# Optimization experiments

Hardware: AMD Instinct MI355X
Metric: run time of the kernel (lower is better)

The kernel has to match this reference:

```python
import jax, jax.numpy as jnp
import numpy as np

B, K = 4, 128
V_IN, V_OUT = 256, 256
E_IN, E_OUT = 512, 512
P_PE, T_PE = 200, 100
HEADS = 16  # c_atten_head


def _lin(key, din, dout):
    kw, kb = jax.random.split(key)
    W = jax.random.normal(kw, (din, dout), jnp.float32) / np.sqrt(din).astype(np.float32)
    b = jax.random.normal(kb, (dout,), jnp.float32) * 0.01
    return W, b


def setup_inputs() -> dict:
    key = jax.random.key(0)
    ks = jax.random.split(key, 14)
    v_f = jax.random.normal(ks[0], (B, K, V_IN), jnp.float32)
    e_f = jax.random.normal(ks[1], (B, K * K, E_IN), jnp.float32)
    p_pe = jax.random.normal(ks[2], (B, K, P_PE), jnp.float32)
    t_pe = jax.random.normal(ks[3], (B, T_PE), jnp.float32)
    e_agg_mask = (jax.random.uniform(ks[4], (B, K, K)) > 0.1).astype(jnp.float32)
    v_agg_mask = (jax.random.uniform(ks[5], (B, K)) > 0.1).astype(jnp.float32)
    W_vpe, b_vpe = _lin(ks[6], V_IN + P_PE + T_PE, V_IN)
    W_epe, b_epe = _lin(ks[7], E_IN + T_PE, E_IN)
    W_ev1, b_ev1 = _lin(ks[8], E_IN + 2 * V_IN, E_OUT)
    W_ev2, b_ev2 = _lin(ks[9], E_OUT, E_OUT)
    W_q, b_q = _lin(ks[10], V_IN, E_OUT)
    W_k, b_k = _lin(ks[11], V_IN, E_OUT)
    W_self, b_self = _lin(ks[12], V_IN, E_OUT)
    W_out, b_out = _lin(ks[13], 2 * E_OUT, V_OUT)
    return dict(v_f=v_f, e_f=e_f, p_pe=p_pe, t_pe=t_pe,
                e_agg_mask=e_agg_mask, v_agg_mask=v_agg_mask,
                W_vpe=W_vpe, b_vpe=b_vpe, W_epe=W_epe, b_epe=b_epe,
                W_ev1=W_ev1, b_ev1=b_ev1, W_ev2=W_ev2, b_ev2=b_ev2,
                W_q=W_q, b_q=b_q, W_k=W_k, b_k=b_k,
                W_self=W_self, b_self=b_self, W_out=W_out, b_out=b_out)


def reference(v_f, e_f, p_pe, t_pe, e_agg_mask, v_agg_mask,
              W_vpe, b_vpe, W_epe, b_epe, W_ev1, b_ev1, W_ev2, b_ev2,
              W_q, b_q, W_k, b_k, W_self, b_self, W_out, b_out):
    silu = jax.nn.silu
    # PE binding
    t_v = jnp.broadcast_to(t_pe[:, None, :], (B, K, T_PE))
    v = silu(jnp.concatenate([v_f, p_pe, t_v], -1) @ W_vpe + b_vpe)          # (B,K,V_IN)
    t_e = jnp.broadcast_to(t_pe[:, None, :], (B, K * K, T_PE))
    e = silu(jnp.concatenate([e_f, t_e], -1) @ W_epe + b_epe)                # (B,K*K,E_IN)
    # dense all-pairs node features -> edge values
    pair = jnp.concatenate([jnp.broadcast_to(v[:, :, None, :], (B, K, K, V_IN)),
                            jnp.broadcast_to(v[:, None, :, :], (B, K, K, V_IN))], -1)
    ev_in = jnp.concatenate([pair.reshape(B, K * K, 2 * V_IN), e], -1)
    e_value = silu(ev_in @ W_ev1 + b_ev1) @ W_ev2 + b_ev2                     # (B,K*K,E_OUT)
    agg_e = e_value.reshape(B, K, K, E_OUT)
    # elementwise-multiply / head-sum attention
    q = v @ W_q + b_q                                                         # (B,K,E_OUT)
    k = v @ W_k + b_k
    att = (q[:, :, None, :] * k[:, None, :, :]).reshape(B, K, K, E_OUT // HEADS, HEADS)
    att = att.sum(-1, keepdims=True) / np.float32(np.sqrt(HEADS * 3.0))       # (B,K,K,G,1)
    a = jax.nn.sigmoid(att) * e_agg_mask[..., None, None]
    a = a / (a.sum(2, keepdims=True) + 1e-6)
    a = jnp.broadcast_to(a, (B, K, K, E_OUT // HEADS, HEADS)).reshape(B, K, K, E_OUT)
    agg_v = (a * agg_e).sum(2)                                                # (B,K,E_OUT)
    v2 = agg_v + silu(v @ W_self + b_self)
    # masked max-pool over nodes
    pooled = (v2 - 1e9 * (1.0 - v_agg_mask)[..., None]).max(1, keepdims=True)
    pooled = jnp.broadcast_to(pooled, (B, K, E_OUT))
    v_out = silu(jnp.concatenate([v2, pooled], -1) @ W_out + b_out)           # (B,K,V_OUT)
    return v_out, e_value
```

## Files before the change

kernel.cpp:

```cpp
#include <hip/hip_runtime.h>

typedef unsigned short ushort_t;
typedef __attribute__((ext_vector_type(8))) short bf16x8;
typedef __attribute__((ext_vector_type(4))) float f32x4;

__device__ __forceinline__ ushort_t f2bf(float f) {
    union { float f; unsigned u; } v; v.f = f;
    unsigned r = v.u + 0x7FFFu + ((v.u >> 16) & 1u);
    return (ushort_t)(r >> 16);
}
__device__ __forceinline__ float siluf(float x) { return x / (1.f + __expf(-x)); }
__device__ __forceinline__ float sigm(float x)  { return 1.f / (1.f + __expf(-x)); }

__device__ __forceinline__ void gl2lds16(const void* g, void* l) {
    __builtin_amdgcn_global_load_lds(
        (__attribute__((address_space(1))) void*)(const_cast<void*>(g)),
        (__attribute__((address_space(3))) void*)(l), 16, 0, 0);
}

__device__ __forceinline__ size_t wts_off(int n, int k) {
    return (size_t)((k >> 5) * 16384) + n * 32
         + ((((k >> 3) & 3) ^ (n & 3)) * 8) + (k & 7);
}

__global__ void k_pt(const float* W_epe, const float* W_ev1, const float* W_ev2,
                     const float* t_pe, const float* W_vpe, const float* b_vpe,
                     const float* b_epe,
                     ushort_t* WT_epe, ushort_t* WT_c, ushort_t* WT_ev2,
                     float* c_v, float* c_e) {
    int n = blockIdx.x, mat = blockIdx.y, t = threadIdx.x;
    if (mat == 3) {
        if (n < 4) {
            int b = n;
            for (int col = t; col < 512; col += 256) {
                float acc = b_epe[col];
                for (int u = 0; u < 100; ++u) acc += t_pe[b*100+u] * W_epe[(512+u)*512 + col];
                c_e[b*512 + col] = acc;
            }
            {
                float acc = b_vpe[t];
                for (int u = 0; u < 100; ++u) acc += t_pe[b*100+u] * W_vpe[(456+u)*256 + t];
                c_v[b*256 + t] = acc;
            }
        }
        return;
    }
    const float* src; ushort_t* dst;
    if (mat == 0)      { src = W_epe;            dst = WT_epe; }
    else if (mat == 1) { src = W_ev1 + 512*512;  dst = WT_c;   }
    else               { src = W_ev2;            dst = WT_ev2; }
    for (int k = t; k < 512; k += 256)
        dst[wts_off(n, k)] = f2bf(src[k*512 + n]);
}

__global__ void k_node_v(const float* v_f, const float* p_pe, const float* W_vpe,
                         const float* c_v, float* v) {
    __shared__ float rv[4][256];
    __shared__ float rp[4][200];
    int r0 = blockIdx.x * 4, t = threadIdx.x;
    for (int rr = 0; rr < 4; ++rr) {
        rv[rr][t] = v_f[(r0+rr)*256 + t];
        if (t < 200) rp[rr][t] = p_pe[(r0+rr)*200 + t];
    }
    __syncthreads();
    int b = r0 >> 7;
    float acc[4];
    float cv = c_v[b*256 + t];
    for (int rr = 0; rr < 4; ++rr) acc[rr] = cv;
    for (int k = 0; k < 256; ++k) {
        float w = W_vpe[k*256 + t];
        #pragma unroll
        for (int rr = 0; rr < 4; ++rr) acc[rr] += rv[rr][k] * w;
    }
    for (int k = 0; k < 200; ++k) {
        float w = W_vpe[(256+k)*256 + t];
        #pragma unroll
        for (int rr = 0; rr < 4; ++rr) acc[rr] += rp[rr][k] * w;
    }
    for (int rr = 0; rr < 4; ++rr) v[(r0+rr)*256 + t] = siluf(acc[rr]);
}

__global__ void k_node_proj(const float* v,
                            const float* W_q, const float* b_q,
                            const float* W_k, const float* b_k,
                            const float* W_self, const float* b_self,
                            const float* W_ev1, const float* b_ev1,
                            float* q, float* kk, float* vs, float* P, float* Q) {
    __shared__ float rv[4][256];
    int r0 = blockIdx.x * 4, which = blockIdx.y, t = threadIdx.x;
    for (int rr = 0; rr < 4; ++rr) rv[rr][t] = v[(r0+rr)*256 + t];
    __syncthreads();
    const float* W; const float* bias = nullptr; float* out; bool do_silu = false;
    if (which == 0)      { W = W_q;    bias = b_q;    out = q;  }
    else if (which == 1) { W = W_k;    bias = b_k;    out = kk; }
    else if (which == 2) { W = W_self; bias = b_self; out = vs; do_silu = true; }
    else if (which == 3) { W = W_ev1;  bias = b_ev1;  out = P;  }
    else                 { W = W_ev1 + 256*512;       out = Q;  }
    float acc[4][2] = {};
    for (int k = 0; k < 256; ++k) {
        float w0 = W[k*512 + t];
        float w1 = W[k*512 + t + 256];
        #pragma unroll
        for (int rr = 0; rr < 4; ++rr) {
            acc[rr][0] += rv[rr][k] * w0;
            acc[rr][1] += rv[rr][k] * w1;
        }
    }
    float bb0 = bias ? bias[t] : 0.f;
    float bb1 = bias ? bias[t + 256] : 0.f;
    for (int rr = 0; rr < 4; ++rr) {
        float x0 = acc[rr][0] + bb0;
        float x1 = acc[rr][1] + bb1;
        if (do_silu) { x0 = siluf(x0); x1 = siluf(x1); }
        out[(r0+rr)*512 + t]       = x0;
        out[(r0+rr)*512 + t + 256] = x1;
    }
}

__global__ __launch_bounds__(256) void k_attw(const float* q, const float* kmat,
                                              const float* emask, float* anorm) {
    int bi = blockIdx.x; int b = bi >> 7, i = bi & 127;
    int t = threadIdx.x;
    __shared__ __align__(16) float qrow[512];
    __shared__ float s[128][33];
    __shared__ float invd[32];
    qrow[t]       = q[(size_t)bi*512 + t];
    qrow[t + 256] = q[(size_t)bi*512 + t + 256];
    __syncthreads();
    {
        int j = t >> 1, g0 = (t & 1) * 16;
        const float* kr = kmat + ((size_t)b*128 + j) * 512;
        float msk = emask[(size_t)b*16384 + i*128 + j];
        for (int gg = 0; gg < 16; ++gg) {
            int g = g0 + gg;
            const float4* k4 = (const float4*)(kr + g*16);
            const float4* q4 = (const float4*)(qrow + g*16);
            float acc = 0.f;
            #pragma unroll
            for (int c = 0; c < 4; ++c) {
                float4 kv = k4[c], qv = q4[c];
                acc += kv.x*qv.x + kv.y*qv.y + kv.z*qv.z + kv.w*qv.w;
            }
            s[j][g] = sigm(acc * 0.14433756729740645f) * msk;
        }
    }
    __syncthreads();
    if (t < 32) {
        float d = 1e-6f;
        for (int j = 0; j < 128; ++j) d += s[j][t];
        invd[t] = 1.f / d;
    }
    __syncthreads();
    float* dst = anorm + (size_t)bi * 4096;
    for (int idx = t; idx < 4096; idx += 256) {
        int j = idx >> 5, g = idx & 31;
        dst[idx] = s[j][g] * invd[g];
    }
}


#define MFMA(A, B, C) __builtin_amdgcn_mfma_f32_16x16x32_bf16((A), (B), (C), 0, 0, 0)

#define ISSUE(W, SL) do {                                                     \
    const ushort_t* wsrc = (W) + (size_t)(SL) * 16384 + wv * 512 + lane * 8;  \
    ushort_t* wdst = bL + ((SL) & 1) * 16384 + wv * 512;                      \
    gl2lds16(wsrc,         wdst);                                             \
    gl2lds16(wsrc + 4096,  wdst + 4096);                                      \
    gl2lds16(wsrc + 8192,  wdst + 8192);                                      \
    gl2lds16(wsrc + 12288, wdst + 12288);                                     \
} while (0)

#define COMPUTE(SL) do {                                                      \
    const ushort_t* sA = aL + (SL) * 2048;                                    \
    const ushort_t* sB = bL + ((SL) & 1) * 16384;                             \
    bf16x8 a0 = *(const bf16x8*)(sA + (ml) * 32 + qs);                        \
    bf16x8 a1 = *(const bf16x8*)(sA + (16 + ml) * 32 + qs);                   \
    bf16x8 a2 = *(const bf16x8*)(sA + (32 + ml) * 32 + qs);                   \
    bf16x8 a3 = *(const bf16x8*)(sA + (48 + ml) * 32 + qs);                   \
    bf16x8 b0 = *(const bf16x8*)(sB + (wn + ml) * 32 + qs);                   \
    bf16x8 b1 = *(const bf16x8*)(sB + (wn + 16 + ml) * 32 + qs);              \
    bf16x8 b2 = *(const bf16x8*)(sB + (wn + 32 + ml) * 32 + qs);              \
    bf16x8 b3 = *(const bf16x8*)(sB + (wn + 48 + ml) * 32 + qs);              \
    acc00 = MFMA(a0, b0, acc00); acc01 = MFMA(a0, b1, acc01);                 \
    acc02 = MFMA(a0, b2, acc02); acc03 = MFMA(a0, b3, acc03);                 \
    acc10 = MFMA(a1, b0, acc10); acc11 = MFMA(a1, b1, acc11);                 \
    acc12 = MFMA(a1, b2, acc12); acc13 = MFMA(a1, b3, acc13);                 \
    acc20 = MFMA(a2, b0, acc20); acc21 = MFMA(a2, b1, acc21);                 \
    acc22 = MFMA(a2, b2, acc22); acc23 = MFMA(a2, b3, acc23);                 \
    acc30 = MFMA(a3, b0, acc30); acc31 = MFMA(a3, b1, acc31);                 \
    acc32 = MFMA(a3, b2, acc32); acc33 = MFMA(a3, b3, acc33);                 \
} while (0)

#define RING(W) do {                                                          \
    for (int sl = 0; sl < 16; ++sl) {                                         \
        if (sl < 15) ISSUE((W), sl + 1);                                      \
        COMPUTE(sl);                                                          \
        __syncthreads();                                                      \
    }                                                                         \
} while (0)

#define EPI0(TM, TN, ACC, CV) {                                               \
    int c  = wn + (TN) * 16 + ml;                                             \
    int cb = (c >> 5) * 2048 + (c & 7);                                       \
    int cx = (c >> 3) & 3;                                                    \
    int j0 = (TM) * 16 + quad * 4;                                            \
    aL[cb + (j0+0)*32 + ((cx ^ 0) * 8)] = f2bf(siluf(ACC[0] + (CV)));         \
    aL[cb + (j0+1)*32 + ((cx ^ 1) * 8)] = f2bf(siluf(ACC[1] + (CV)));         \
    aL[cb + (j0+2)*32 + ((cx ^ 2) * 8)] = f2bf(siluf(ACC[2] + (CV)));         \
    aL[cb + (j0+3)*32 + ((cx ^ 3) * 8)] = f2bf(siluf(ACC[3] + (CV)));         \
    ACC = zero4; }

#define EPI1(TM, TN, ACC, PV) {                                               \
    int c  = wn + (TN) * 16 + ml;                                             \
    int cb = (c >> 5) * 2048 + (c & 7);                                       \
    int cx = (c >> 3) & 3;                                                    \
    int j0 = (TM) * 16 + quad * 4;                                            \
    const float* qp = Qbuf + (size_t)(b_ * 128 + half * 64 + j0) * 512 + c;   \
    aL[cb + (j0+0)*32 + ((cx ^ 0) * 8)] = f2bf(siluf(ACC[0] + (PV) + qp[0]));    \
    aL[cb + (j0+1)*32 + ((cx ^ 1) * 8)] = f2bf(siluf(ACC[1] + (PV) + qp[512]));  \
    aL[cb + (j0+2)*32 + ((cx ^ 2) * 8)] = f2bf(siluf(ACC[2] + (PV) + qp[1024])); \
    aL[cb + (j0+3)*32 + ((cx ^ 3) * 8)] = f2bf(siluf(ACC[3] + (PV) + qp[1536])); \
    ACC = zero4; }

#define EPI2(TM, TN, ACC, BV, PART) {                                         \
    int c  = wn + (TN) * 16 + ml;                                             \
    int g  = c >> 4;                                                          \
    int j0 = (TM) * 16 + quad * 4;                                            \
    float* op = out_e + (size_t)(r0 + j0) * 512 + c;                          \
    float x0 = ACC[0] + (BV); op[0]    = x0; PART += awl[(j0+0)*32 + g] * x0; \
    float x1 = ACC[1] + (BV); op[512]  = x1; PART += awl[(j0+1)*32 + g] * x1; \
    float x2 = ACC[2] + (BV); op[1024] = x2; PART += awl[(j0+2)*32 + g] * x2; \
    float x3 = ACC[3] + (BV); op[1536] = x3; PART += awl[(j0+3)*32 + g] * x3; }

__global__ __launch_bounds__(512) void k_chain(const float* ef,
                                               const ushort_t* W0, const ushort_t* W1,
                                               const ushort_t* W2,
                                               const float* c_e, const float* Pbuf,
                                               const float* Qbuf, const float* b_ev2,
                                               const float* anorm,
                                               float* out_e, float* v2buf) {
    __shared__ __align__(16) ushort_t smem[65536];
    int lin = blockIdx.x;
    int mt = (lin & 7) * 128 + (lin >> 3);
    int r0 = mt * 64;
    int bi = mt >> 1;
    int b_ = mt >> 8;
    int half = mt & 1;
    int t = threadIdx.x;
    int wv = t >> 6, lane = t & 63;
    int wn = wv * 64;
    int ml = lane & 15, quad = lane >> 4;
    int qs = (quad ^ (ml & 3)) * 8;

    const f32x4 zero4 = {0.f, 0.f, 0.f, 0.f};
    f32x4 acc00 = zero4, acc01 = zero4, acc02 = zero4, acc03 = zero4;
    f32x4 acc10 = zero4, acc11 = zero4, acc12 = zero4, acc13 = zero4;
    f32x4 acc20 = zero4, acc21 = zero4, acc22 = zero4, acc23 = zero4;
    f32x4 acc30 = zero4, acc31 = zero4, acc32 = zero4, acc33 = zero4;

    ushort_t* aL = smem;
    ushort_t* bL = smem + 32768;

    ISSUE(W0, 0);
    for (int i = 0; i < 16; ++i) {
        int qd  = i * 512 + t;
        int row = qd >> 7, k4 = (qd & 127) * 4;
        float4 f4 = *(const float4*)(ef + (size_t)(r0 + row) * 512 + k4);
        ushort_t* d = aL + (k4 >> 5) * 2048 + row * 32
                    + ((((k4 >> 3) & 3) ^ (row & 3)) * 8) + (k4 & 7);
        *(ushort4*)d = make_ushort4(f2bf(f4.x), f2bf(f4.y), f2bf(f4.z), f2bf(f4.w));
    }
    __syncthreads();
    RING(W0);
    {
        float cv0 = c_e[b_ * 512 + wn +  0 + ml];
        float cv1 = c_e[b_ * 512 + wn + 16 + ml];
        float cv2 = c_e[b_ * 512 + wn + 32 + ml];
        float cv3 = c_e[b_ * 512 + wn + 48 + ml];
        EPI0(0,0,acc00,cv0) EPI0(0,1,acc01,cv1) EPI0(0,2,acc02,cv2) EPI0(0,3,acc03,cv3)
        EPI0(1,0,acc10,cv0) EPI0(1,1,acc11,cv1) EPI0(1,2,acc12,cv2) EPI0(1,3,acc13,cv3)
        EPI0(2,0,acc20,cv0) EPI0(2,1,acc21,cv1) EPI0(2,2,acc22,cv2) EPI0(2,3,acc23,cv3)
        EPI0(3,0,acc30,cv0) EPI0(3,1,acc31,cv1) EPI0(3,2,acc32,cv2) EPI0(3,3,acc33,cv3)
    }
    ISSUE(W1, 0);
    __syncthreads();
    RING(W1);
    {
        float Pv0 = Pbuf[(size_t)bi * 512 + wn +  0 + ml];
        float Pv1 = Pbuf[(size_t)bi * 512 + wn + 16 + ml];
        float Pv2 = Pbuf[(size_t)bi * 512 + wn + 32 + ml];
        float Pv3 = Pbuf[(size_t)bi * 512 + wn + 48 + ml];
        EPI1(0,0,acc00,Pv0) EPI1(0,1,acc01,Pv1) EPI1(0,2,acc02,Pv2) EPI1(0,3,acc03,Pv3)
        EPI1(1,0,acc10,Pv0) EPI1(1,1,acc11,Pv1) EPI1(1,2,acc12,Pv2) EPI1(1,3,acc13,Pv3)
        EPI1(2,0,acc20,Pv0) EPI1(2,1,acc21,Pv1) EPI1(2,2,acc22,Pv2) EPI1(2,3,acc23,Pv3)
        EPI1(3,0,acc30,Pv0) EPI1(3,1,acc31,Pv1) EPI1(3,2,acc32,Pv2) EPI1(3,3,acc33,Pv3)
    }
    ISSUE(W2, 0);
    __syncthreads();
    RING(W2);
    {
        float* awl = (float*)bL;
        ((float4*)awl)[t] = ((const float4*)(anorm + (size_t)bi * 4096 + half * 2048))[t];
        __syncthreads();
        float bv0 = b_ev2[wn +  0 + ml];
        float bv1 = b_ev2[wn + 16 + ml];
        float bv2 = b_ev2[wn + 32 + ml];
        float bv3 = b_ev2[wn + 48 + ml];
        float p0 = 0.f, p1 = 0.f, p2 = 0.f, p3 = 0.f;
        EPI2(0,0,acc00,bv0,p0) EPI2(0,1,acc01,bv1,p1) EPI2(0,2,acc02,bv2,p2) EPI2(0,3,acc03,bv3,p3)
        EPI2(1,0,acc10,bv0,p0) EPI2(1,1,acc11,bv1,p1) EPI2(1,2,acc12,bv2,p2) EPI2(1,3,acc13,bv3,p3)
        EPI2(2,0,acc20,bv0,p0) EPI2(2,1,acc21,bv1,p1) EPI2(2,2,acc22,bv2,p2) EPI2(2,3,acc23,bv3,p3)
        EPI2(3,0,acc30,bv0,p0) EPI2(3,1,acc31,bv1,p1) EPI2(3,2,acc32,bv2,p2) EPI2(3,3,acc33,bv3,p3)
        { float p = p0; p += __shfl_down(p, 32); p += __shfl_down(p, 16);
          if (lane < 16) atomicAdd(v2buf + (size_t)bi * 512 + wn +  0 + ml, p); }
        { float p = p1; p += __shfl_down(p, 32); p += __shfl_down(p, 16);
          if (lane < 16) atomicAdd(v2buf + (size_t)bi * 512 + wn + 16 + ml, p); }
        { float p = p2; p += __shfl_down(p, 32); p += __shfl_down(p, 16);
          if (lane < 16) atomicAdd(v2buf + (size_t)bi * 512 + wn + 32 + ml, p); }
        { float p = p3; p += __shfl_down(p, 32); p += __shfl_down(p, 16);
          if (lane < 16) atomicAdd(v2buf + (size_t)bi * 512 + wn + 48 + ml, p); }
    }
}

__global__ __launch_bounds__(1024) void k_out(const float* v2, const float* vmask,
                                              const float* W_out, const float* b_out,
                                              float* out) {
    __shared__ float rv[2][512];
    __shared__ float vm[128];
    __shared__ float pm[2][512];
    __shared__ float pooled[512];
    __shared__ float red[2][2][256];
    __shared__ float cpred[2][256];
    int t = threadIdx.x;
    int r0 = blockIdx.x * 2, b = r0 >> 7;
    if (t < 128) vm[t] = -1e9f * (1.f - vmask[b*128 + t]);
    rv[t >> 9][t & 511] = v2[(size_t)(r0 + (t >> 9)) * 512 + (t & 511)];
    __syncthreads();
    {
        int col = t & 511, rc = t >> 9;
        int i0 = rc * 64;
        const float* src = v2 + ((size_t)(b*128 + i0)) * 512 + col;
        float m = -1e30f;
        #pragma unroll 8
        for (int i = 0; i < 64; ++i)
            m = fmaxf(m, src[(size_t)i * 512] + vm[i0 + i]);
        pm[rc][col] = m;
    }
    __syncthreads();
    if (t < 512) pooled[t] = fmaxf(pm[0][t], pm[1][t]);
    __syncthreads();
    {
        int col = t & 255, kc = t >> 8;
        if (kc < 2) {
            int k0 = kc * 256;
            float a0 = 0.f, a1 = 0.f;
            #pragma unroll 8
            for (int k = 0; k < 256; ++k) {
                float w = W_out[(size_t)(k0 + k) * 256 + col];
                a0 += rv[0][k0 + k] * w;
                a1 += rv[1][k0 + k] * w;
            }
            red[kc][0][col] = a0;
            red[kc][1][col] = a1;
        } else {
            int d0 = (kc - 2) * 256;
            float cp = 0.f;
            #pragma unroll 8
            for (int d = 0; d < 256; ++d)
                cp += pooled[d0 + d] * W_out[(size_t)(512 + d0 + d) * 256 + col];
            cpred[kc - 2][col] = cp;
        }
    }
    __syncthreads();
    if (t < 512) {
        int row = t >> 8, c = t & 255;
        float x = red[0][row][c] + red[1][row][c]
                + cpred[0][c] + cpred[1][c] + b_out[c];
        out[(size_t)(r0 + row) * 256 + c] = siluf(x);
    }
}

extern "C" void kernel_launch(void* const* d_in, const int* in_sizes, int n_in,
                              void* d_out, int out_size, void* d_ws, size_t ws_size,
                              hipStream_t stream) {
    const float* v_f    = (const float*)d_in[0];
    const float* e_f    = (const float*)d_in[1];
    const float* p_pe   = (const float*)d_in[2];
    const float* t_pe   = (const float*)d_in[3];
    const float* emask  = (const float*)d_in[4];
    const float* vmask  = (const float*)d_in[5];
    const float* W_vpe  = (const float*)d_in[6];
    const float* b_vpe  = (const float*)d_in[7];
    const float* W_epe  = (const float*)d_in[8];
    const float* b_epe  = (const float*)d_in[9];
    const float* W_ev1  = (const float*)d_in[10];
    const float* b_ev1  = (const float*)d_in[11];
    const float* W_ev2  = (const float*)d_in[12];
    const float* b_ev2  = (const float*)d_in[13];
    const float* W_q    = (const float*)d_in[14];
    const float* b_q    = (const float*)d_in[15];
    const float* W_k    = (const float*)d_in[16];
    const float* b_k    = (const float*)d_in[17];
    const float* W_self = (const float*)d_in[18];
    const float* b_self = (const float*)d_in[19];
    const float* W_out  = (const float*)d_in[20];
    const float* b_out  = (const float*)d_in[21];

    float* out_v = (float*)d_out;
    float* out_e = (float*)d_out + 131072;

    char* w = (char*)d_ws;
    ushort_t* WT_epe = (ushort_t*)w; w += 512*512*2;
    ushort_t* WT_c   = (ushort_t*)w; w += 512*512*2;
    ushort_t* WT_ev2 = (ushort_t*)w; w += 512*512*2;
    float* c_v   = (float*)w; w += 4*256*4;
    float* c_e   = (float*)w; w += 4*512*4;
    float* v     = (float*)w; w += 512*256*4;
    float* qbuf  = (float*)w; w += 512*512*4;
    float* kbuf  = (float*)w; w += 512*512*4;
    float* Pbuf  = (float*)w; w += 512*512*4;
    float* Qbuf  = (float*)w; w += 512*512*4;
    float* v2buf = (float*)w; w += 512*512*4;
    float* anorm = (float*)w; w += (size_t)4*128*128*32*4;

    k_pt<<<dim3(512, 4), 256, 0, stream>>>(W_epe, W_ev1, W_ev2, t_pe, W_vpe, b_vpe, b_epe,
                                           WT_epe, WT_c, WT_ev2, c_v, c_e);
    k_node_v<<<128, 256, 0, stream>>>(v_f, p_pe, W_vpe, c_v, v);
    k_node_proj<<<dim3(128, 5), 256, 0, stream>>>(v, W_q, b_q, W_k, b_k, W_self, b_self,
                                                  W_ev1, b_ev1, qbuf, kbuf, v2buf, Pbuf, Qbuf);
    k_attw<<<512, 256, 0, stream>>>(qbuf, kbuf, emask, anorm);
    k_chain<<<1024, 512, 0, stream>>>(e_f, WT_epe, WT_c, WT_ev2, c_e, Pbuf, Qbuf,
                                      b_ev2, anorm, out_e, v2buf);
    k_out<<<256, 1024, 0, stream>>>(v2buf, vmask, W_out, b_out, out_v);
}
```

Before: 593.7 us.

## Deepen k_chain weight prefetch ring and coalesce weight transpose via LDS

The k_chain GEMM ring now keeps two weight slices in flight, using explicit vmcnt waits, raw barriers and s_setprio around the MFMA compute, so global-to-LDS loads overlap with more compute. The weight transpose/bf16 pack kernel is reorganised to stage a 32xK tile in shared memory and write coalesced ushort4 stores, which cuts its grid from 512 to 32 blocks per matrix. The per-batch time-embedding bias work moves into one block. The hand-written waitcnt logic depends on how many loads ISSUE emits and risks races if that count is wrong.

Result: slower. 610.9 us (+2.9%).

```diff
diff --git a/kernel.cpp b/kernel.cpp
--- a/kernel.cpp
+++ b/kernel.cpp
@@ -23,21 +23,21 @@
          + ((((k >> 3) & 3) ^ (n & 3)) * 8) + (k & 7);
 }
 
-__global__ void k_pt(const float* W_epe, const float* W_ev1, const float* W_ev2,
+__global__ __launch_bounds__(256) void k_pt(const float* W_epe, const float* W_ev1,
+                     const float* W_ev2,
                      const float* t_pe, const float* W_vpe, const float* b_vpe,
                      const float* b_epe,
                      ushort_t* WT_epe, ushort_t* WT_c, ushort_t* WT_ev2,
                      float* c_v, float* c_e) {
-    int n = blockIdx.x, mat = blockIdx.y, t = threadIdx.x;
+    int mat = blockIdx.y, t = threadIdx.x;
     if (mat == 3) {
-        if (n < 4) {
-            int b = n;
-            for (int col = t; col < 512; col += 256) {
-                float acc = b_epe[col];
-                for (int u = 0; u < 100; ++u) acc += t_pe[b*100+u] * W_epe[(512+u)*512 + col];
-                c_e[b*512 + col] = acc;
-            }
-            {
+        if (blockIdx.x == 0) {
+            for (int b = 0; b < 4; ++b) {
+                for (int col = t; col < 512; col += 256) {
+                    float acc = b_epe[col];
+                    for (int u = 0; u < 100; ++u) acc += t_pe[b*100+u] * W_epe[(512+u)*512 + col];
+                    c_e[b*512 + col] = acc;
+                }
                 float acc = b_vpe[t];
                 for (int u = 0; u < 100; ++u) acc += t_pe[b*100+u] * W_vpe[(456+u)*256 + t];
                 c_v[b*256 + t] = acc;
@@ -49,8 +49,18 @@
     if (mat == 0)      { src = W_epe;            dst = WT_epe; }
     else if (mat == 1) { src = W_ev1 + 512*512;  dst = WT_c;   }
     else               { src = W_ev2;            dst = WT_ev2; }
-    for (int k = t; k < 512; k += 256)
-        dst[wts_off(n, k)] = f2bf(src[k*512 + n]);
+    __shared__ ushort_t lds[8192];
+    int ks = blockIdx.x >> 1, n0 = (blockIdx.x & 1) * 256;
+    for (int kk = 0; kk < 32; ++kk) {
+        float v = src[(size_t)(ks * 32 + kk) * 512 + n0 + t];
+        lds[t * 32 + ((((kk >> 3) & 3) ^ (t & 3)) * 8) + (kk & 7)] = f2bf(v);
+    }
+    __syncthreads();
+    ushort4* gd = (ushort4*)(dst + (size_t)ks * 16384 + n0 * 32);
+    const ushort4* ls = (const ushort4*)lds;
+    #pragma unroll
+    for (int it = 0; it < 8; ++it)
+        gd[it * 256 + t] = ls[it * 256 + t];
 }
 
 __global__ void k_node_v(const float* v_f, const float* p_pe, const float* W_vpe,
@@ -192,10 +202,17 @@
 } while (0)
 
 #define RING(W) do {                                                          \
+    _Pragma("unroll")                                                         \
     for (int sl = 0; sl < 16; ++sl) {                                         \
-        if (sl < 15) ISSUE((W), sl + 1);                                      \
+        if (sl < 15) { asm volatile("s_waitcnt vmcnt(4)" ::: "memory"); }     \
+        else         { asm volatile("s_waitcnt vmcnt(0)" ::: "memory"); }     \
+        __builtin_amdgcn_s_barrier();        \
+        __builtin_amdgcn_s_setprio(1);                                        \
         COMPUTE(sl);                                                          \
-        __syncthreads();                                                      \
+        __builtin_amdgcn_s_setprio(0);                                        \
+        asm volatile("s_waitcnt lgkmcnt(0)" ::: "memory");                    \
+        __builtin_amdgcn_s_barrier();                     \
+        if (sl < 14) ISSUE((W), sl + 2);                                      \
     }                                                                         \
 } while (0)
 
@@ -261,7 +278,7 @@
     ushort_t* aL = smem;
     ushort_t* bL = smem + 32768;
 
-    ISSUE(W0, 0);
+    ISSUE(W0, 0); ISSUE(W0, 1);
     for (int i = 0; i < 16; ++i) {
         int qd  = i * 512 + t;
         int row = qd >> 7, k4 = (qd & 127) * 4;
@@ -270,7 +287,7 @@
                     + ((((k4 >> 3) & 3) ^ (row & 3)) * 8) + (k4 & 7);
         *(ushort4*)d = make_ushort4(f2bf(f4.x), f2bf(f4.y), f2bf(f4.z), f2bf(f4.w));
     }
-    __syncthreads();
+    asm volatile("s_waitcnt lgkmcnt(0)" ::: "memory");
     RING(W0);
     {
         float cv0 = c_e[b_ * 512 + wn +  0 + ml];
@@ -282,8 +299,8 @@
         EPI0(2,0,acc20,cv0) EPI0(2,1,acc21,cv1) EPI0(2,2,acc22,cv2) EPI0(2,3,acc23,cv3)
         EPI0(3,0,acc30,cv0) EPI0(3,1,acc31,cv1) EPI0(3,2,acc32,cv2) EPI0(3,3,acc33,cv3)
     }
-    ISSUE(W1, 0);
-    __syncthreads();
+    ISSUE(W1, 0); ISSUE(W1, 1);
+    asm volatile("s_waitcnt lgkmcnt(0)" ::: "memory");
     RING(W1);
     {
         float Pv0 = Pbuf[(size_t)bi * 512 + wn +  0 + ml];
@@ -295,8 +312,8 @@
         EPI1(2,0,acc20,Pv0) EPI1(2,1,acc21,Pv1) EPI1(2,2,acc22,Pv2) EPI1(2,3,acc23,Pv3)
         EPI1(3,0,acc30,Pv0) EPI1(3,1,acc31,Pv1) EPI1(3,2,acc32,Pv2) EPI1(3,3,acc33,Pv3)
     }
-    ISSUE(W2, 0);
-    __syncthreads();
+    ISSUE(W2, 0); ISSUE(W2, 1);
+    asm volatile("s_waitcnt lgkmcnt(0)" ::: "memory");
     RING(W2);
     {
         float* awl = (float*)bL;
@@ -423,8 +440,8 @@
     float* v2buf = (float*)w; w += 512*512*4;
     float* anorm = (float*)w; w += (size_t)4*128*128*32*4;
 
-    k_pt<<<dim3(512, 4), 256, 0, stream>>>(W_epe, W_ev1, W_ev2, t_pe, W_vpe, b_vpe, b_epe,
-                                           WT_epe, WT_c, WT_ev2, c_v, c_e);
+    k_pt<<<dim3(32, 4), 256, 0, stream>>>(W_epe, W_ev1, W_ev2, t_pe, W_vpe, b_vpe, b_epe,
+                                          WT_epe, WT_c, WT_ev2, c_v, c_e);
     k_node_v<<<128, 256, 0, stream>>>(v_f, p_pe, W_vpe, c_v, v);
     k_node_proj<<<dim3(128, 5), 256, 0, stream>>>(v, W_q, b_q, W_k, b_k, W_self, b_self,
                                                   W_ev1, b_ev1, qbuf, kbuf, v2buf, Pbuf, Qbuf);
```
